# Optimization experiments

Hardware: AMD Instinct MI355X
Metric: run time of the kernel (lower is better)

## Reference

```python
import jax, jax.numpy as jnp
import numpy as np

DIM = 1024
NUM_HEADS = 32
HEAD_DIM = 32
T = 2048
SCALE = 0.12
ROT_BASE = HEAD_DIM * 4  # Rotary(head_dim, max_seq_len, head_dim*4)
RMS_EPS = 1.1920929e-07  # torch float32 finfo eps (F.rms_norm default)


def _rms_norm(x):
    ms = jnp.mean(jnp.square(x), axis=-1, keepdims=True)
    return x * jax.lax.rsqrt(ms + RMS_EPS)


def _rotary_tables(seq_len):
    # modded-nanogpt half-truncated rotary: frequencies on first quarter, zeros on second
    quarter = HEAD_DIM // 4
    af = (1.0 / ROT_BASE) ** jnp.linspace(0.0, 1.0, quarter, dtype=jnp.float32)
    af = jnp.concatenate([af, jnp.zeros(quarter, dtype=jnp.float32)])  # [hd/2]
    theta = jnp.arange(seq_len, dtype=jnp.float32)[:, None] * af[None, :]  # [T, hd/2]
    return jnp.cos(theta), jnp.sin(theta)


def _apply_rotary(x, cos, sin):
    # x: [B, T, H, hd]; cos/sin: [T, hd/2]
    x1, x2 = jnp.split(x, 2, axis=-1)
    c = cos[None, :, None, :]
    s = sin[None, :, None, :]
    y1 = x1 * c + x2 * s
    y2 = -x1 * s + x2 * c
    return jnp.concatenate([y1, y2], axis=-1)


def setup_inputs() -> dict:
    key = jax.random.key(0)
    k1, k2, k3, k4 = jax.random.split(key, 4)
    std = 0.5 * DIM ** (-0.5)
    bound = (3.0 ** 0.5) * std
    x = jax.random.normal(k1, (1, T, DIM), dtype=jnp.float32)
    ve = jax.random.normal(k2, (1, T, NUM_HEADS * HEAD_DIM), dtype=jnp.float32)
    qkv_w = jax.random.uniform(k3, (3, NUM_HEADS * HEAD_DIM, DIM), dtype=jnp.float32,
                               minval=-bound, maxval=bound)
    lambdas = jnp.array([0.5, 0.5], dtype=jnp.float32)
    # original zero-inits c_proj; use small random so output/grads are nontrivial
    c_proj_w = jax.random.normal(k4, (DIM, NUM_HEADS * HEAD_DIM), dtype=jnp.float32) * 0.02
    return {"x": x, "ve": ve, "qkv_w": qkv_w, "lambdas": lambdas, "c_proj_w": c_proj_w}


def reference(x, ve, qkv_w, lambdas, c_proj_w):
    B, T_, D = x.shape
    H, hd = NUM_HEADS, HEAD_DIM
    # fused QKV projection: F.linear(x, qkv_w.flatten(end_dim=1))
    w = qkv_w.reshape(3 * H * hd, D)
    qkv = jnp.einsum('btd,ed->bte', x, w).reshape(B, T_, 3 * H, hd)
    q, k, v = jnp.split(qkv, 3, axis=2)  # each [B, T, H, hd]
    q = _rms_norm(q)
    k = _rms_norm(k)
    cos, sin = _rotary_tables(T_)
    q = _apply_rotary(q, cos, sin)
    k = _apply_rotary(k, cos, sin)
    v = lambdas[0] * v + lambdas[1] * ve.reshape(B, T_, H, hd)
    # causal attention with fixed scale 0.12
    scores = jnp.einsum('bqhd,bkhd->bhqk', q, k) * SCALE
    causal = jnp.tril(jnp.ones((T_, T_), dtype=bool))
    scores = jnp.where(causal[None, None, :, :], scores, -jnp.inf)
    attn = jax.nn.softmax(scores, axis=-1)
    y = jnp.einsum('bhqk,bkhd->bqhd', attn, v).reshape(B, T_, H * hd)
    return jnp.einsum('bte,de->btd', y, c_proj_w)
```

## Files before the change

kernel.cpp:

```cpp
#include <hip/hip_runtime.h>
#include <hip/hip_bf16.h>

#define NHEADS 32
#define HD_ 32
#define TSEQ 2048
#define SCALE_ 0.12f
#define LOG2E_ 1.44269504088896f
#define RMS_EPS_ 1.1920929e-07f

typedef unsigned short ushort_t;
typedef __bf16 bf16_t;
typedef __attribute__((ext_vector_type(8))) bf16_t bf16x8;
typedef __attribute__((ext_vector_type(4))) float f32x4;
typedef __attribute__((ext_vector_type(8))) unsigned short u16x8;

__device__ __forceinline__ ushort_t f2bfn(float f){
    __hip_bfloat16 b = __float2bfloat16(f);
    return *reinterpret_cast<ushort_t*>(&b);
}
__device__ __forceinline__ float bf2f(ushort_t s){
    union { unsigned u; float f; } v; v.u = ((unsigned)s) << 16;
    return v.f;
}
__device__ __forceinline__ float fexp2(float x){
#if __has_builtin(__builtin_amdgcn_exp2f)
    return __builtin_amdgcn_exp2f(x);
#else
    return exp2f(x);
#endif
}
__device__ __forceinline__ void gld16(const void* g, void* l){
    __builtin_amdgcn_global_load_lds(
        (const __attribute__((address_space(1))) unsigned int*)g,
        (__attribute__((address_space(3))) unsigned int*)l,
        16, 0, 0);
}

__global__ __launch_bounds__(256) void k_convert(const float* __restrict__ src,
                                                 ushort_t* __restrict__ dst, int n4){
    int i = blockIdx.x * blockDim.x + threadIdx.x;
    int stride = gridDim.x * blockDim.x;
    for (; i < n4; i += stride){
        float4 v = ((const float4*)src)[i];
        ushort4 o;
        o.x = f2bfn(v.x); o.y = f2bfn(v.y); o.z = f2bfn(v.z); o.w = f2bfn(v.w);
        ((ushort4*)dst)[i] = o;
    }
}

__global__ __launch_bounds__(256) void k_tables(float* __restrict__ cost, float* __restrict__ sint){
    int gid = blockIdx.x * 256 + threadIdx.x;
    if (gid >= TSEQ * 16) return;
    int t = gid >> 4, i = gid & 15;
    float c = 1.0f, s = 0.0f;
    if (i < 8){
        float af = powf(1.0f / 128.0f, (float)i * (1.0f / 7.0f));
        float th = (float)t * af;
        sincosf(th, &s, &c);
    }
    cost[gid] = c;
    sint[gid] = s;
}

template<int BN, bool OUT_BF16>
__global__ __launch_bounds__(256) void k_gemm_bt(const ushort_t* __restrict__ A,
                                                 const ushort_t* __restrict__ B,
                                                 void* __restrict__ C,
                                                 int M, int N, int K)
{
    constexpr int NF = BN / 32;
    __shared__ __align__(16) ushort_t As[128 * 32];
    __shared__ __align__(16) ushort_t Bs[BN * 32];
    const int tid = threadIdx.x;
    const int lane = tid & 63;
    const int w = tid >> 6;
    const int wr = w >> 1, wc = w & 1;
    const int l15 = lane & 15, hi = lane >> 4;
    const int m0 = blockIdx.y * 128, n0 = blockIdx.x * BN;
    const int srow = lane >> 2, skc = (lane & 3) * 8;

    f32x4 acc[4][NF] = {};

    for (int k0 = 0; k0 < K; k0 += 32){
        __syncthreads();
        #pragma unroll
        for (int i = 0; i < 2; ++i){
            int c = w * 2 + i;
            gld16(&A[(size_t)(m0 + c * 16 + srow) * K + k0 + skc], &As[c * 512]);
        }
        #pragma unroll
        for (int i = 0; i < BN / 64; ++i){
            int c = w * (BN / 64) + i;
            gld16(&B[(size_t)(n0 + c * 16 + srow) * K + k0 + skc], &Bs[c * 512]);
        }
        __syncthreads();
        bf16x8 af[4], bfr[NF];
        #pragma unroll
        for (int mi = 0; mi < 4; ++mi)
            af[mi] = *(const bf16x8*)&As[(wr * 64 + mi * 16 + l15) * 32 + hi * 8];
        #pragma unroll
        for (int ni = 0; ni < NF; ++ni)
            bfr[ni] = *(const bf16x8*)&Bs[(wc * (BN / 2) + ni * 16 + l15) * 32 + hi * 8];
        #pragma unroll
        for (int mi = 0; mi < 4; ++mi)
            #pragma unroll
            for (int ni = 0; ni < NF; ++ni)
                acc[mi][ni] = __builtin_amdgcn_mfma_f32_16x16x32_bf16(af[mi], bfr[ni], acc[mi][ni], 0, 0, 0);
    }

    #pragma unroll
    for (int mi = 0; mi < 4; ++mi){
        #pragma unroll
        for (int ni = 0; ni < NF; ++ni){
            #pragma unroll
            for (int r = 0; r < 4; ++r){
                int row = m0 + wr * 64 + mi * 16 + hi * 4 + r;
                int col = n0 + wc * (BN / 2) + ni * 16 + l15;
                float v = acc[mi][ni][r];
                if (OUT_BF16) ((ushort_t*)C)[(size_t)row * N + col] = f2bfn(v);
                else          ((float*)C)[(size_t)row * N + col] = v;
            }
        }
    }
}

__global__ __launch_bounds__(256) void k_fuse(const ushort_t* __restrict__ qkvb,
                                              const float* __restrict__ ve,
                                              const float* __restrict__ lam,
                                              const float* __restrict__ cost,
                                              const float* __restrict__ sint,
                                              ushort_t* __restrict__ qb,
                                              ushort_t* __restrict__ kb,
                                              ushort_t* __restrict__ vtb)
{
    const int h  = blockIdx.y;
    const int t0 = blockIdx.x * 64;
    const int tid = threadIdx.x;
    const int tl = tid >> 2;
    const int dg = tid & 3;
    const int t  = t0 + tl;

    __shared__ __align__(16) float vtile[32 * 65];

    float cs[8], sn[8];
    #pragma unroll
    for (int j = 0; j < 8; ++j){
        int ci = (dg * 8 + j) & 15;
        cs[j] = cost[t * 16 + ci];
        sn[j] = sint[t * 16 + ci];
    }
    const float sgn = (dg < 2) ? 1.0f : -1.0f;

    #pragma unroll
    for (int which = 0; which < 2; ++which){
        u16x8 raw = *(const u16x8*)&qkvb[(size_t)t * 3072 + which * 1024 + h * 32 + dg * 8];
        float v[8];
        float ss = 0.0f;
        #pragma unroll
        for (int j = 0; j < 8; ++j){ v[j] = bf2f(raw[j]); ss += v[j] * v[j]; }
        ss += __shfl_xor(ss, 1);
        ss += __shfl_xor(ss, 2);
        const float inv = rsqrtf(ss * (1.0f / 32.0f) + RMS_EPS_);
        const float scl = (which == 0) ? SCALE_ * LOG2E_ : 1.0f;
        u16x8 o;
        #pragma unroll
        for (int j = 0; j < 8; ++j){
            float nv = v[j] * inv;
            float p  = __shfl_xor(nv, 2);
            o[j] = f2bfn((nv * cs[j] + sgn * p * sn[j]) * scl);
        }
        ushort_t* dst = (which == 0) ? qb : kb;
        *(u16x8*)&dst[((size_t)h * TSEQ + t) * 32 + dg * 8] = o;
    }

    const float l0 = lam[0], l1 = lam[1];
    {
        u16x8 raw = *(const u16x8*)&qkvb[(size_t)t * 3072 + 2048 + h * 32 + dg * 8];
        const float4* vep = (const float4*)&ve[(size_t)t * 1024 + h * 32 + dg * 8];
        float4 a = vep[0], b = vep[1];
        float vef[8] = {a.x, a.y, a.z, a.w, b.x, b.y, b.z, b.w};
        #pragma unroll
        for (int j = 0; j < 8; ++j)
            vtile[(dg * 8 + j) * 65 + tl] = l0 * bf2f(raw[j]) + l1 * vef[j];
    }
    __syncthreads();
    {
        const int d = tid >> 3, jj = tid & 7;
        u16x8 o;
        #pragma unroll
        for (int e = 0; e < 8; ++e)
            o[e] = f2bfn(vtile[d * 65 + jj * 8 + e]);
        *(u16x8*)&vtb[((size_t)h * HD_ + d) * TSEQ + t0 + jj * 8] = o;
    }
}

template<bool MASK>
__device__ __forceinline__ void attn_tile(const ushort_t* __restrict__ kb,
                                          const ushort_t* __restrict__ vtb,
                                          ushort_t* pb, const bf16x8& q_frag,
                                          int h, int kb0, int qw, int l15, int hi,
                                          f32x4& acc0, f32x4& acc1, float* m, float* lp)
{
    bf16x8 vv0[2], vv1[2];
    #pragma unroll
    for (int kk = 0; kk < 2; ++kk){
        vv0[kk] = *(const bf16x8*)&vtb[((size_t)h * HD_ + l15) * TSEQ + kb0 + kk * 32 + hi * 8];
        vv1[kk] = *(const bf16x8*)&vtb[((size_t)h * HD_ + 16 + l15) * TSEQ + kb0 + kk * 32 + hi * 8];
    }
    f32x4 s[4];
    #pragma unroll
    for (int ni = 0; ni < 4; ++ni){
        bf16x8 kf = *(const bf16x8*)&kb[((size_t)h * TSEQ + kb0 + ni * 16 + l15) * 32 + hi * 8];
        f32x4 z = {0.f, 0.f, 0.f, 0.f};
        s[ni] = __builtin_amdgcn_mfma_f32_16x16x32_bf16(q_frag, kf, z, 0, 0, 0);
    }
    if (MASK){
        #pragma unroll
        for (int ni = 0; ni < 4; ++ni){
            int col = kb0 + ni * 16 + l15;
            #pragma unroll
            for (int r = 0; r < 4; ++r)
                if (col > qw + hi * 4 + r) s[ni][r] = -1e30f;
        }
    }
    float sc[4];
    #pragma unroll
    for (int r = 0; r < 4; ++r){
        float mt = fmaxf(fmaxf(s[0][r], s[1][r]), fmaxf(s[2][r], s[3][r]));
        mt = fmaxf(mt, __shfl_xor(mt, 1));
        mt = fmaxf(mt, __shfl_xor(mt, 2));
        mt = fmaxf(mt, __shfl_xor(mt, 4));
        mt = fmaxf(mt, __shfl_xor(mt, 8));
        float mn = fmaxf(m[r], mt);
        sc[r] = fexp2(m[r] - mn);
        m[r] = mn;
    }
    #pragma unroll
    for (int r = 0; r < 4; ++r){
        float ps = 0.f;
        #pragma unroll
        for (int ni = 0; ni < 4; ++ni){
            float p = fexp2(s[ni][r] - m[r]);
            s[ni][r] = p;
            ps += p;
        }
        lp[r] = lp[r] * sc[r] + ps;
        acc0[r] *= sc[r];
        acc1[r] *= sc[r];
    }
    #pragma unroll
    for (int ni = 0; ni < 4; ++ni)
        #pragma unroll
        for (int r = 0; r < 4; ++r)
            pb[(hi * 4 + r) * 72 + ni * 16 + l15] = f2bfn(s[ni][r]);
    #pragma unroll
    for (int kk = 0; kk < 2; ++kk){
        bf16x8 pf = *(const bf16x8*)&pb[l15 * 72 + kk * 32 + hi * 8];
        acc0 = __builtin_amdgcn_mfma_f32_16x16x32_bf16(pf, vv0[kk], acc0, 0, 0, 0);
        acc1 = __builtin_amdgcn_mfma_f32_16x16x32_bf16(pf, vv1[kk], acc1, 0, 0, 0);
    }
}

__global__ __launch_bounds__(256) void k_attn(const ushort_t* __restrict__ qb,
                                              const ushort_t* __restrict__ kb,
                                              const ushort_t* __restrict__ vtb,
                                              ushort_t* __restrict__ yb)
{
    const int h  = blockIdx.y;
    const int tid = threadIdx.x;
    const int w = tid >> 6, lane = tid & 63;
    const int l15 = lane & 15, hi = lane >> 4;

    __shared__ __align__(16) ushort_t Pbuf[4][16 * 72];
    ushort_t* pb = &Pbuf[w][0];

    for (int half = 0; half < 2; ++half){
        const int qt = half ? (31 - (int)blockIdx.x) : (int)blockIdx.x;
        const int qw = qt * 64 + w * 16;
        const bf16x8 q_frag = *(const bf16x8*)&qb[((size_t)h * TSEQ + qw + l15) * 32 + hi * 8];

        f32x4 acc0 = {0.f, 0.f, 0.f, 0.f}, acc1 = {0.f, 0.f, 0.f, 0.f};
        float m[4]  = {-1e30f, -1e30f, -1e30f, -1e30f};
        float lp[4] = {0.f, 0.f, 0.f, 0.f};

        for (int kt = 0; kt < qt; ++kt)
            attn_tile<false>(kb, vtb, pb, q_frag, h, kt * 64, qw, l15, hi, acc0, acc1, m, lp);
        attn_tile<true>(kb, vtb, pb, q_frag, h, qt * 64, qw, l15, hi, acc0, acc1, m, lp);

        #pragma unroll
        for (int r = 0; r < 4; ++r){
            float ls = lp[r];
            ls += __shfl_xor(ls, 1);
            ls += __shfl_xor(ls, 2);
            ls += __shfl_xor(ls, 4);
            ls += __shfl_xor(ls, 8);
            float inv = 1.0f / ls;
            int row = qw + hi * 4 + r;
            yb[(size_t)row * 1024 + h * 32 + l15]      = f2bfn(acc0[r] * inv);
            yb[(size_t)row * 1024 + h * 32 + 16 + l15] = f2bfn(acc1[r] * inv);
        }
    }
}

extern "C" void kernel_launch(void* const* d_in, const int* in_sizes, int n_in,
                              void* d_out, int out_size, void* d_ws, size_t ws_size,
                              hipStream_t stream)
{
    const float* x   = (const float*)d_in[0];
    const float* ve  = (const float*)d_in[1];
    const float* qkw = (const float*)d_in[2];
    const float* lam = (const float*)d_in[3];
    const float* cpw = (const float*)d_in[4];

    char* ws = (char*)d_ws;
    size_t o = 0;
    auto take = [&](size_t bytes) -> char* {
        char* p = ws + o; o += (bytes + 255) & ~(size_t)255; return p;
    };
    ushort_t* xb   = (ushort_t*)take((size_t)TSEQ * 1024 * 2);
    ushort_t* wb   = (ushort_t*)take((size_t)3072 * 1024 * 2);
    ushort_t* cpb  = (ushort_t*)take((size_t)1024 * 1024 * 2);
    ushort_t* qkvb = (ushort_t*)take((size_t)TSEQ * 3072 * 2);
    float*    cost = (float*)take((size_t)TSEQ * 16 * 4);
    float*    sint = (float*)take((size_t)TSEQ * 16 * 4);
    ushort_t* qb   = (ushort_t*)take((size_t)NHEADS * TSEQ * HD_ * 2);
    ushort_t* kb   = (ushort_t*)take((size_t)NHEADS * TSEQ * HD_ * 2);
    ushort_t* vtb  = (ushort_t*)take((size_t)NHEADS * HD_ * TSEQ * 2);
    ushort_t* yb   = xb;

    k_convert<<<512, 256, 0, stream>>>(x,   xb,  TSEQ * 1024 / 4);
    k_convert<<<768, 256, 0, stream>>>(qkw, wb,  3072 * 1024 / 4);
    k_convert<<<256, 256, 0, stream>>>(cpw, cpb, 1024 * 1024 / 4);
    k_tables<<<TSEQ * 16 / 256, 256, 0, stream>>>(cost, sint);
    k_gemm_bt<128, true ><<<dim3(3072 / 128, TSEQ / 128), 256, 0, stream>>>(xb, wb, qkvb, TSEQ, 3072, 1024);
    k_fuse<<<dim3(TSEQ / 64, NHEADS), 256, 0, stream>>>(qkvb, ve, lam, cost, sint, qb, kb, vtb);
    k_attn<<<dim3(16, NHEADS), 256, 0, stream>>>(qb, kb, vtb, yb);
    k_gemm_bt<64, false><<<dim3(1024 / 64, TSEQ / 128), 256, 0, stream>>>(yb, cpb, (float*)d_out, TSEQ, 1024, 1024);
}
```

Baseline: 190.0 us.

## Split attention KV range across two wave groups and retile GEMMs with K=64

The attention kernel now runs 512 threads per block. Two groups of four waves each process half of the key tiles for the same query tiles, and their online-softmax states are merged through shared memory. The QK and PV MFMAs swap operand order so each lane owns one query row, which removes the 16-lane shuffle reductions and allows vectorized P and output stores. Both GEMMs move to a 64-deep K step with smaller M tiles (64 rows), which doubles the block count and halves the number of barrier iterations. The costs are more shared memory, an extra merge and barrier in attention, and smaller GEMM tiles with less reuse.

Measured after the change: 182.0 us. 1.04x faster.

```diff
diff --git a/kernel.cpp b/kernel.cpp
--- a/kernel.cpp
+++ b/kernel.cpp
@@ -62,66 +62,70 @@
     sint[gid] = s;
 }
 
-template<int BN, bool OUT_BF16>
-__global__ __launch_bounds__(256) void k_gemm_bt(const ushort_t* __restrict__ A,
-                                                 const ushort_t* __restrict__ B,
-                                                 void* __restrict__ C,
-                                                 int M, int N, int K)
-{
-    constexpr int NF = BN / 32;
-    __shared__ __align__(16) ushort_t As[128 * 32];
-    __shared__ __align__(16) ushort_t Bs[BN * 32];
+template<int BM, int BN, bool OUT_BF16>
+__global__ __launch_bounds__(256) void k_gemm64(const ushort_t* __restrict__ A,
+                                                const ushort_t* __restrict__ B,
+                                                void* __restrict__ C,
+                                                int M, int N, int K)
+{
+    constexpr int MI = BM / 32, NI = BN / 32;
+    __shared__ __align__(16) ushort_t As[BM * 64];
+    __shared__ __align__(16) ushort_t Bs[BN * 64];
     const int tid = threadIdx.x;
     const int lane = tid & 63;
     const int w = tid >> 6;
     const int wr = w >> 1, wc = w & 1;
     const int l15 = lane & 15, hi = lane >> 4;
-    const int m0 = blockIdx.y * 128, n0 = blockIdx.x * BN;
-    const int srow = lane >> 2, skc = (lane & 3) * 8;
-
-    f32x4 acc[4][NF] = {};
-
-    for (int k0 = 0; k0 < K; k0 += 32){
+    const int m0 = blockIdx.y * BM, n0 = blockIdx.x * BN;
+    const int srow = lane >> 3, scol = (lane & 7) * 8;
+
+    f32x4 acc[MI][NI] = {};
+
+    for (int k0 = 0; k0 < K; k0 += 64){
         __syncthreads();
         #pragma unroll
-        for (int i = 0; i < 2; ++i){
-            int c = w * 2 + i;
-            gld16(&A[(size_t)(m0 + c * 16 + srow) * K + k0 + skc], &As[c * 512]);
+        for (int i = 0; i < BM / 32; ++i){
+            int c = w * (BM / 32) + i;
+            gld16(&A[(size_t)(m0 + c * 8 + srow) * K + k0 + scol], &As[c * 512]);
         }
         #pragma unroll
-        for (int i = 0; i < BN / 64; ++i){
-            int c = w * (BN / 64) + i;
-            gld16(&B[(size_t)(n0 + c * 16 + srow) * K + k0 + skc], &Bs[c * 512]);
+        for (int i = 0; i < BN / 32; ++i){
+            int c = w * (BN / 32) + i;
+            gld16(&B[(size_t)(n0 + c * 8 + srow) * K + k0 + scol], &Bs[c * 512]);
         }
         __syncthreads();
-        bf16x8 af[4], bfr[NF];
-        #pragma unroll
-        for (int mi = 0; mi < 4; ++mi)
-            af[mi] = *(const bf16x8*)&As[(wr * 64 + mi * 16 + l15) * 32 + hi * 8];
-        #pragma unroll
-        for (int ni = 0; ni < NF; ++ni)
-            bfr[ni] = *(const bf16x8*)&Bs[(wc * (BN / 2) + ni * 16 + l15) * 32 + hi * 8];
-        #pragma unroll
-        for (int mi = 0; mi < 4; ++mi)
+        bf16x8 af[MI][2], bfr[NI][2];
+        #pragma unroll
+        for (int mi = 0; mi < MI; ++mi)
             #pragma unroll
-            for (int ni = 0; ni < NF; ++ni)
-                acc[mi][ni] = __builtin_amdgcn_mfma_f32_16x16x32_bf16(af[mi], bfr[ni], acc[mi][ni], 0, 0, 0);
-    }
-
-    #pragma unroll
-    for (int mi = 0; mi < 4; ++mi){
-        #pragma unroll
-        for (int ni = 0; ni < NF; ++ni){
+            for (int sub = 0; sub < 2; ++sub)
+                af[mi][sub] = *(const bf16x8*)&As[(wr * (BM/2) + mi * 16 + l15) * 64 + sub * 32 + hi * 8];
+        #pragma unroll
+        for (int ni = 0; ni < NI; ++ni)
+            #pragma unroll
+            for (int sub = 0; sub < 2; ++sub)
+                bfr[ni][sub] = *(const bf16x8*)&Bs[(wc * (BN/2) + ni * 16 + l15) * 64 + sub * 32 + hi * 8];
+        #pragma unroll
+        for (int sub = 0; sub < 2; ++sub)
+            #pragma unroll
+            for (int mi = 0; mi < MI; ++mi)
+                #pragma unroll
+                for (int ni = 0; ni < NI; ++ni)
+                    acc[mi][ni] = __builtin_amdgcn_mfma_f32_16x16x32_bf16(af[mi][sub], bfr[ni][sub], acc[mi][ni], 0, 0, 0);
+    }
+
+    #pragma unroll
+    for (int mi = 0; mi < MI; ++mi)
+        #pragma unroll
+        for (int ni = 0; ni < NI; ++ni)
             #pragma unroll
             for (int r = 0; r < 4; ++r){
-                int row = m0 + wr * 64 + mi * 16 + hi * 4 + r;
-                int col = n0 + wc * (BN / 2) + ni * 16 + l15;
+                int row = m0 + wr * (BM/2) + mi * 16 + hi * 4 + r;
+                int col = n0 + wc * (BN/2) + ni * 16 + l15;
                 float v = acc[mi][ni][r];
                 if (OUT_BF16) ((ushort_t*)C)[(size_t)row * N + col] = f2bfn(v);
                 else          ((float*)C)[(size_t)row * N + col] = v;
             }
-        }
-    }
 }
 
 __global__ __launch_bounds__(256) void k_fuse(const ushort_t* __restrict__ qkvb,
@@ -194,110 +198,168 @@
     }
 }
 
+struct ChainState { f32x4 a0, a1; float m, lp; };
+
 template<bool MASK>
-__device__ __forceinline__ void attn_tile(const ushort_t* __restrict__ kb,
-                                          const ushort_t* __restrict__ vtb,
-                                          ushort_t* pb, const bf16x8& q_frag,
-                                          int h, int kb0, int qw, int l15, int hi,
-                                          f32x4& acc0, f32x4& acc1, float* m, float* lp)
+__device__ __forceinline__ void attn_tile(const ushort_t* __restrict__ kb_h,
+                                          const ushort_t* __restrict__ vt_h,
+                                          ushort_t* pb, const bf16x8& qf,
+                                          int kb0, int qglob, int l15, int hi,
+                                          ChainState& st)
 {
     bf16x8 vv0[2], vv1[2];
     #pragma unroll
     for (int kk = 0; kk < 2; ++kk){
-        vv0[kk] = *(const bf16x8*)&vtb[((size_t)h * HD_ + l15) * TSEQ + kb0 + kk * 32 + hi * 8];
-        vv1[kk] = *(const bf16x8*)&vtb[((size_t)h * HD_ + 16 + l15) * TSEQ + kb0 + kk * 32 + hi * 8];
+        vv0[kk] = *(const bf16x8*)&vt_h[(size_t)l15 * TSEQ + kb0 + kk * 32 + hi * 8];
+        vv1[kk] = *(const bf16x8*)&vt_h[(size_t)(16 + l15) * TSEQ + kb0 + kk * 32 + hi * 8];
     }
     f32x4 s[4];
     #pragma unroll
     for (int ni = 0; ni < 4; ++ni){
-        bf16x8 kf = *(const bf16x8*)&kb[((size_t)h * TSEQ + kb0 + ni * 16 + l15) * 32 + hi * 8];
+        bf16x8 kf = *(const bf16x8*)&kb_h[(size_t)(kb0 + ni * 16 + l15) * 32 + hi * 8];
         f32x4 z = {0.f, 0.f, 0.f, 0.f};
-        s[ni] = __builtin_amdgcn_mfma_f32_16x16x32_bf16(q_frag, kf, z, 0, 0, 0);
+        s[ni] = __builtin_amdgcn_mfma_f32_16x16x32_bf16(kf, qf, z, 0, 0, 0);
     }
     if (MASK){
         #pragma unroll
-        for (int ni = 0; ni < 4; ++ni){
-            int col = kb0 + ni * 16 + l15;
+        for (int ni = 0; ni < 4; ++ni)
             #pragma unroll
             for (int r = 0; r < 4; ++r)
-                if (col > qw + hi * 4 + r) s[ni][r] = -1e30f;
-        }
-    }
-    float sc[4];
-    #pragma unroll
-    for (int r = 0; r < 4; ++r){
-        float mt = fmaxf(fmaxf(s[0][r], s[1][r]), fmaxf(s[2][r], s[3][r]));
-        mt = fmaxf(mt, __shfl_xor(mt, 1));
-        mt = fmaxf(mt, __shfl_xor(mt, 2));
-        mt = fmaxf(mt, __shfl_xor(mt, 4));
-        mt = fmaxf(mt, __shfl_xor(mt, 8));
-        float mn = fmaxf(m[r], mt);
-        sc[r] = fexp2(m[r] - mn);
-        m[r] = mn;
-    }
-    #pragma unroll
-    for (int r = 0; r < 4; ++r){
-        float ps = 0.f;
-        #pragma unroll
-        for (int ni = 0; ni < 4; ++ni){
-            float p = fexp2(s[ni][r] - m[r]);
+                if (kb0 + ni * 16 + hi * 4 + r > qglob) s[ni][r] = -1e30f;
+    }
+    float mt = -1e30f;
+    #pragma unroll
+    for (int ni = 0; ni < 4; ++ni)
+        #pragma unroll
+        for (int r = 0; r < 4; ++r)
+            mt = fmaxf(mt, s[ni][r]);
+    mt = fmaxf(mt, __shfl_xor(mt, 16));
+    mt = fmaxf(mt, __shfl_xor(mt, 32));
+    float mn = fmaxf(st.m, mt);
+    float sc = fexp2(st.m - mn);
+    st.m = mn;
+    float ps = 0.f;
+    #pragma unroll
+    for (int ni = 0; ni < 4; ++ni)
+        #pragma unroll
+        for (int r = 0; r < 4; ++r){
+            float p = fexp2(s[ni][r] - mn);
             s[ni][r] = p;
             ps += p;
         }
-        lp[r] = lp[r] * sc[r] + ps;
-        acc0[r] *= sc[r];
-        acc1[r] *= sc[r];
-    }
-    #pragma unroll
-    for (int ni = 0; ni < 4; ++ni)
-        #pragma unroll
-        for (int r = 0; r < 4; ++r)
-            pb[(hi * 4 + r) * 72 + ni * 16 + l15] = f2bfn(s[ni][r]);
+    st.lp = st.lp * sc + ps;
+    #pragma unroll
+    for (int r = 0; r < 4; ++r){ st.a0[r] *= sc; st.a1[r] *= sc; }
+    #pragma unroll
+    for (int ni = 0; ni < 4; ++ni){
+        ushort4 pk;
+        pk.x = f2bfn(s[ni][0]); pk.y = f2bfn(s[ni][1]);
+        pk.z = f2bfn(s[ni][2]); pk.w = f2bfn(s[ni][3]);
+        *(ushort4*)&pb[l15 * 72 + ni * 16 + hi * 4] = pk;
+    }
     #pragma unroll
     for (int kk = 0; kk < 2; ++kk){
         bf16x8 pf = *(const bf16x8*)&pb[l15 * 72 + kk * 32 + hi * 8];
-        acc0 = __builtin_amdgcn_mfma_f32_16x16x32_bf16(pf, vv0[kk], acc0, 0, 0, 0);
-        acc1 = __builtin_amdgcn_mfma_f32_16x16x32_bf16(pf, vv1[kk], acc1, 0, 0, 0);
-    }
-}
-
-__global__ __launch_bounds__(256) void k_attn(const ushort_t* __restrict__ qb,
-                                              const ushort_t* __restrict__ kb,
-                                              const ushort_t* __restrict__ vtb,
-                                              ushort_t* __restrict__ yb)
+        st.a0 = __builtin_amdgcn_mfma_f32_16x16x32_bf16(vv0[kk], pf, st.a0, 0, 0, 0);
+        st.a1 = __builtin_amdgcn_mfma_f32_16x16x32_bf16(vv1[kk], pf, st.a1, 0, 0, 0);
+    }
+}
+
+__device__ __forceinline__ void run_range(const ushort_t* kb_h, const ushort_t* vt_h,
+                                          ushort_t* pb, const bf16x8& qf, int qglob,
+                                          int lo, int hi_t, int nT, int l15, int hi,
+                                          ChainState& st)
+{
+    int stop = (hi_t < nT) ? hi_t : (nT - 1);
+    for (int kt = lo; kt < stop; ++kt)
+        attn_tile<false>(kb_h, vt_h, pb, qf, kt * 64, qglob, l15, hi, st);
+    if (hi_t == nT && lo < nT)
+        attn_tile<true>(kb_h, vt_h, pb, qf, (nT - 1) * 64, qglob, l15, hi, st);
+}
+
+__device__ __forceinline__ void merge_state(ChainState& s, const float* mb){
+    float m2 = mb[0];
+    float mn = fmaxf(s.m, m2);
+    float f1 = fexp2(s.m - mn), f2 = fexp2(m2 - mn);
+    s.lp = s.lp * f1 + mb[1] * f2;
+    #pragma unroll
+    for (int r = 0; r < 4; ++r){
+        s.a0[r] = s.a0[r] * f1 + mb[2 + r] * f2;
+        s.a1[r] = s.a1[r] * f1 + mb[6 + r] * f2;
+    }
+    s.m = mn;
+}
+
+__global__ __launch_bounds__(512, 4) void k_attn(const ushort_t* __restrict__ qb,
+                                                 const ushort_t* __restrict__ kb,
+                                                 const ushort_t* __restrict__ vtb,
+                                                 ushort_t* __restrict__ yb)
 {
     const int h  = blockIdx.y;
+    const int b  = blockIdx.x;
     const int tid = threadIdx.x;
     const int w = tid >> 6, lane = tid & 63;
+    const int ws = w & 3, half2 = w >> 2;
     const int l15 = lane & 15, hi = lane >> 4;
 
-    __shared__ __align__(16) ushort_t Pbuf[4][16 * 72];
-    ushort_t* pb = &Pbuf[w][0];
-
-    for (int half = 0; half < 2; ++half){
-        const int qt = half ? (31 - (int)blockIdx.x) : (int)blockIdx.x;
-        const int qw = qt * 64 + w * 16;
-        const bf16x8 q_frag = *(const bf16x8*)&qb[((size_t)h * TSEQ + qw + l15) * 32 + hi * 8];
-
-        f32x4 acc0 = {0.f, 0.f, 0.f, 0.f}, acc1 = {0.f, 0.f, 0.f, 0.f};
-        float m[4]  = {-1e30f, -1e30f, -1e30f, -1e30f};
-        float lp[4] = {0.f, 0.f, 0.f, 0.f};
-
-        for (int kt = 0; kt < qt; ++kt)
-            attn_tile<false>(kb, vtb, pb, q_frag, h, kt * 64, qw, l15, hi, acc0, acc1, m, lp);
-        attn_tile<true>(kb, vtb, pb, q_frag, h, qt * 64, qw, l15, hi, acc0, acc1, m, lp);
-
-        #pragma unroll
-        for (int r = 0; r < 4; ++r){
-            float ls = lp[r];
-            ls += __shfl_xor(ls, 1);
-            ls += __shfl_xor(ls, 2);
-            ls += __shfl_xor(ls, 4);
-            ls += __shfl_xor(ls, 8);
+    __shared__ __align__(16) ushort_t Pall[8][16 * 72];
+    __shared__ float mbuf[4][64][20];
+    ushort_t* pb = &Pall[w][0];
+
+    const ushort_t* kb_h = kb + (size_t)h * TSEQ * HD_;
+    const ushort_t* vt_h = vtb + (size_t)h * HD_ * TSEQ;
+    const ushort_t* qb_h = qb + (size_t)h * TSEQ * HD_;
+
+    const int qtA = b, qtB = 31 - b;
+    const int nA = qtA + 1, nB = qtB + 1;
+    const int hA = (nA + 1) >> 1, hB = nB >> 1;
+
+    const int qwA = qtA * 64 + ws * 16;
+    const int qwB = qtB * 64 + ws * 16;
+    const bf16x8 qfA = *(const bf16x8*)&qb_h[(size_t)(qwA + l15) * 32 + hi * 8];
+    const bf16x8 qfB = *(const bf16x8*)&qb_h[(size_t)(qwB + l15) * 32 + hi * 8];
+
+    ChainState stA, stB;
+    stA.a0 = {0.f,0.f,0.f,0.f}; stA.a1 = {0.f,0.f,0.f,0.f}; stA.m = -1e30f; stA.lp = 0.f;
+    stB = stA;
+
+    if (half2 == 0){
+        run_range(kb_h, vt_h, pb, qfA, qwA + l15, 0, hA, nA, l15, hi, stA);
+        run_range(kb_h, vt_h, pb, qfB, qwB + l15, 0, hB, nB, l15, hi, stB);
+    } else {
+        run_range(kb_h, vt_h, pb, qfA, qwA + l15, hA, nA, nA, l15, hi, stA);
+        run_range(kb_h, vt_h, pb, qfB, qwB + l15, hB, nB, nB, l15, hi, stB);
+    }
+
+    if (half2 == 1){
+        float* mb = &mbuf[ws][lane][0];
+        mb[0] = stA.m; mb[1] = stA.lp;
+        #pragma unroll
+        for (int r = 0; r < 4; ++r){ mb[2 + r] = stA.a0[r]; mb[6 + r] = stA.a1[r]; }
+        mb[10] = stB.m; mb[11] = stB.lp;
+        #pragma unroll
+        for (int r = 0; r < 4; ++r){ mb[12 + r] = stB.a0[r]; mb[16 + r] = stB.a1[r]; }
+    }
+    __syncthreads();
+    if (half2 == 0){
+        merge_state(stA, &mbuf[ws][lane][0]);
+        merge_state(stB, &mbuf[ws][lane][10]);
+        #pragma unroll
+        for (int which = 0; which < 2; ++which){
+            ChainState& st = which ? stB : stA;
+            int qw = which ? qwB : qwA;
+            float ls = st.lp;
+            ls += __shfl_xor(ls, 16);
+            ls += __shfl_xor(ls, 32);
             float inv = 1.0f / ls;
-            int row = qw + hi * 4 + r;
-            yb[(size_t)row * 1024 + h * 32 + l15]      = f2bfn(acc0[r] * inv);
-            yb[(size_t)row * 1024 + h * 32 + 16 + l15] = f2bfn(acc1[r] * inv);
+            ushort4 o0, o1;
+            o0.x = f2bfn(st.a0[0]*inv); o0.y = f2bfn(st.a0[1]*inv);
+            o0.z = f2bfn(st.a0[2]*inv); o0.w = f2bfn(st.a0[3]*inv);
+            o1.x = f2bfn(st.a1[0]*inv); o1.y = f2bfn(st.a1[1]*inv);
+            o1.z = f2bfn(st.a1[2]*inv); o1.w = f2bfn(st.a1[3]*inv);
+            size_t base = (size_t)(qw + l15) * 1024 + h * 32;
+            *(ushort4*)&yb[base + hi * 4]      = o0;
+            *(ushort4*)&yb[base + 16 + hi * 4] = o1;
         }
     }
 }
@@ -332,8 +394,8 @@
     k_convert<<<768, 256, 0, stream>>>(qkw, wb,  3072 * 1024 / 4);
     k_convert<<<256, 256, 0, stream>>>(cpw, cpb, 1024 * 1024 / 4);
     k_tables<<<TSEQ * 16 / 256, 256, 0, stream>>>(cost, sint);
-    k_gemm_bt<128, true ><<<dim3(3072 / 128, TSEQ / 128), 256, 0, stream>>>(xb, wb, qkvb, TSEQ, 3072, 1024);
+    k_gemm64<64, 128, true ><<<dim3(3072 / 128, TSEQ / 64), 256, 0, stream>>>(xb, wb, qkvb, TSEQ, 3072, 1024);
     k_fuse<<<dim3(TSEQ / 64, NHEADS), 256, 0, stream>>>(qkvb, ve, lam, cost, sint, qb, kb, vtb);
-    k_attn<<<dim3(16, NHEADS), 256, 0, stream>>>(qb, kb, vtb, yb);
-    k_gemm_bt<64, false><<<dim3(1024 / 64, TSEQ / 128), 256, 0, stream>>>(yb, cpb, (float*)d_out, TSEQ, 1024, 1024);
-}
+    k_attn<<<dim3(16, NHEADS), 512, 0, stream>>>(qb, kb, vtb, yb);
+    k_gemm64<64, 64, false><<<dim3(1024 / 64, TSEQ / 64), 256, 0, stream>>>(yb, cpb, (float*)d_out, TSEQ, 1024, 1024);
+}
```
